# Optimization experiments

Hardware: AMD Instinct MI355X
Metric: run time of the kernel (lower is better)

Reference implementation:

```python
import jax, jax.numpy as jnp
import numpy as np

D = 512   # embed_dim
K = 8     # expand_dim
TAU = 16.0
LN_EPS = 1e-5


def setup_inputs() -> dict:
    key = jax.random.key(0)
    ks = jax.random.split(key, 8)
    b, n = 4, 4096
    x = jax.random.normal(ks[0], (b, n, D), dtype=jnp.float32)
    # nn.Linear weights stored as (in, out); bias=False everywhere
    W_i = jax.random.normal(ks[1], (D, D), dtype=jnp.float32) / np.sqrt(D)
    W_e = jax.random.normal(ks[2], (D, K), dtype=jnp.float32) / np.sqrt(D)
    W_s = jax.random.normal(ks[3], (D, K), dtype=jnp.float32) / np.sqrt(D)
    o_param = jax.random.normal(ks[4], (K, D), dtype=jnp.float32) * 0.1
    ln_gamma = jnp.ones((D,), dtype=jnp.float32)
    ln_beta = jnp.zeros((D,), dtype=jnp.float32)
    W_out = jax.random.normal(ks[5], (D, D), dtype=jnp.float32) / np.sqrt(D)
    return {"x": x, "W_i": W_i, "W_e": W_e, "W_s": W_s, "o_param": o_param,
            "ln_gamma": ln_gamma, "ln_beta": ln_beta, "W_out": W_out}


def reference(x, W_i, W_e, W_s, o_param, ln_gamma, ln_beta, W_out):
    b, n, d = x.shape
    k = W_e.shape[1]
    i = x @ W_i            # (b,n,d) input branch
    e = x @ W_e            # (b,n,k) expand branch (t_type=0: identity)
    s = x @ W_s            # (b,n,k) shrink branch
    # data-independent decay gate: exp(logsigmoid(o)/tau), shape (k,d)
    o = jnp.exp(jax.nn.log_sigmoid(o_param) / TAU)

    def step(m, inp):
        it, et, st = inp          # (b,d), (b,k), (b,k)
        m = o * m + et[:, :, None] * it[:, None, :]   # (b,k,d)
        y = jnp.einsum('bk,bkd->bd', st, m)
        return m, y

    m0 = jnp.zeros((b, k, d), dtype=x.dtype)
    xs = (jnp.swapaxes(i, 0, 1), jnp.swapaxes(e, 0, 1), jnp.swapaxes(s, 0, 1))
    _, ys = jax.lax.scan(step, m0, xs)   # ys: (n,b,d)
    y = jnp.swapaxes(ys, 0, 1)           # (b,n,d)
    # LayerNorm
    mu = jnp.mean(y, axis=-1, keepdims=True)
    var = jnp.mean(jnp.square(y - mu), axis=-1, keepdims=True)
    y = (y - mu) * jax.lax.rsqrt(var + LN_EPS) * ln_gamma + ln_beta
    return y @ W_out
```

## Files before the change

kernel.cpp:

```cpp
#include <hip/hip_runtime.h>
#include <stdint.h>

typedef __bf16 bf16;
typedef __bf16 bf16x8 __attribute__((ext_vector_type(8)));
typedef float  f32x4  __attribute__((ext_vector_type(4)));

#define NSEQ 4096
#define NROWS 16384
#define CHUNK 32
#define NCHUNKS_B 128
#define NCHUNKS 512
#define SEGLEN 16
#define NSEG 8
#define YSTRIDE 516

__device__ __forceinline__ float bf2f(uint16_t u){
    uint32_t w = ((uint32_t)u) << 16;
    return __builtin_bit_cast(float, w);
}
__device__ __forceinline__ uint32_t pack2(float a, float b){
    uint16_t ua = __builtin_bit_cast(uint16_t, (bf16)a);
    uint16_t ub = __builtin_bit_cast(uint16_t, (bf16)b);
    return ((uint32_t)ub << 16) | (uint32_t)ua;
}
__device__ __forceinline__ uint4 cvt8(const float* p){
    float4 lo = *(const float4*)p;
    float4 hi = *(const float4*)(p + 4);
    uint4 r;
    r.x = pack2(lo.x, lo.y); r.y = pack2(lo.z, lo.w);
    r.z = pack2(hi.x, hi.y); r.w = pack2(hi.z, hi.w);
    return r;
}
__device__ __forceinline__ float rd_any(const void* p, long idx, int f){
    return f ? ((const float*)p)[idx] : (float)((const bf16*)p)[idx];
}
__device__ __forceinline__ void cp16(const void* g, void* l){
    __builtin_amdgcn_global_load_lds((const __attribute__((address_space(1))) void*)g,
                                     (__attribute__((address_space(3))) void*)l,
                                     16, 0, 0);
}

__global__ __launch_bounds__(256) void prep_kernel(const uint32_t* __restrict__ xw,
                                                   const void* We, const void* Ws,
                                                   const void* op, const void* g, const void* b,
                                                   bf16* __restrict__ Wt_es,
                                                   float* __restrict__ g_c, float* __restrict__ b_c,
                                                   float* __restrict__ o_buf, float* __restrict__ oL_buf,
                                                   float* __restrict__ lsL_buf, float* __restrict__ oL16_buf,
                                                   int* __restrict__ flag_g){
    __shared__ int cnt[256];
    int tid = threadIdx.x;
    int c = 0;
    #pragma unroll
    for (int j = 0; j < 4; ++j){
        uint32_t w = xw[tid*4 + j];
        uint32_t e = (w >> 7) & 0xFF;
        c += (e >= 110 && e <= 140) ? 1 : 0;
    }
    cnt[tid] = c; __syncthreads();
    for (int s = 128; s; s >>= 1){
        if (tid < s) cnt[tid] += cnt[tid + s];
        __syncthreads();
    }
    int f = (cnt[0] < 512) ? 1 : 0;
    int blk = blockIdx.x;
    if (blk == 0 && tid == 0) flag_g[0] = f;
    if (blk < 8){
        for (int i = tid; i < 1024; i += 256){
            int gi = blk*1024 + i;
            int n = gi >> 9, k = gi & 511;
            float v = (n < 8) ? rd_any(We, (long)k*8 + n, f)
                              : rd_any(Ws, (long)k*8 + (n-8), f);
            Wt_es[gi] = (bf16)v;
        }
    } else {
        int base = (blk - 8) * 1024;
        for (int i = tid; i < 1024; i += 256){
            int gi = base + i;
            float x = rd_any(op, gi, f);
            float ls = (x < 0.f) ? (x - log1pf(expf(x))) : (0.f - log1pf(expf(-x)));
            o_buf[gi]    = expf(ls * (1.0f/16.0f));
            oL_buf[gi]   = expf(ls * 2.0f);
            lsL_buf[gi]  = ls * 2.0f;
            oL16_buf[gi] = expf(ls * 32.0f);
        }
    }
    if (blk == 0){
        for (int i = tid; i < 512; i += 256){
            g_c[i] = rd_any(g, i, f);
            b_c[i] = rd_any(b, i, f);
        }
    }
}

__global__ __launch_bounds__(256) void transpose2(const void* __restrict__ Wi,
                                                  const void* __restrict__ Wo,
                                                  bf16* __restrict__ Wt_i,
                                                  bf16* __restrict__ Wt_o,
                                                  const int* __restrict__ flag){
    __shared__ bf16 T[64][65];
    int mat = blockIdx.x >> 6;
    int t   = blockIdx.x & 63;
    int k0  = (t >> 3) * 64, n0 = (t & 7) * 64;
    const void* in = mat ? Wo : Wi;
    bf16* out = mat ? Wt_o : Wt_i;
    int f = *flag;
    int tid = threadIdx.x;
    #pragma unroll
    for (int e = 0; e < 16; ++e){
        int idx = e*256 + tid;
        int r = idx >> 6, c = idx & 63;
        T[c][r] = (bf16)rd_any(in, (long)(k0 + r)*512 + n0 + c, f);
    }
    __syncthreads();
    #pragma unroll
    for (int e = 0; e < 16; ++e){
        int idx = e*256 + tid;
        int rn = idx >> 6, ck = idx & 63;
        out[(long)(n0 + rn)*512 + k0 + ck] = T[rn][ck];
    }
}

__global__ __launch_bounds__(256) void gemm_bt(const void* __restrict__ Avoid,
                                               const bf16* __restrict__ Bt,
                                               void* __restrict__ Cvoid,
                                               int M, int N, int Kd,
                                               const int* __restrict__ aflag,
                                               const int* __restrict__ cflag,
                                               const bf16* __restrict__ Wes,
                                               float* __restrict__ e_out,
                                               float* __restrict__ s_out){
    __shared__ __align__(16) bf16 As[128*32];
    __shared__ __align__(16) bf16 Bs[128*32];
    const int tid  = threadIdx.x;
    const int lane = tid & 63;
    const int wave = tid >> 6;
    const int ntiles = N >> 7;
    int bid = blockIdx.x;
    {
        const int q = gridDim.x >> 3;
        bid = (bid & 7) * q + (bid >> 3);
    }
    const int mtile = bid / ntiles;
    const int ntile = bid - mtile*ntiles;
    const int m0 = mtile << 7, n0 = ntile << 7;
    const int wr = (wave >> 1) << 6;
    const int wc = (wave & 1) << 6;
    const int lrow = lane & 15;
    const int quad = lane >> 4;
    const int fa = aflag ? *aflag : 0;
    const bool do_es = (Wes != nullptr) && (ntile == 0) && (wc == 0);

    f32x4 acc[4][4] = {};
    f32x4 acc_es[4] = {};

    const int sr = tid >> 2;
    const int sk = (tid & 3) << 3;
    const bf16*  Ag  = (const bf16*) Avoid + (long)(m0 + sr)*Kd + sk;
    const float* Agf = (const float*)Avoid + (long)(m0 + sr)*Kd + sk;
    const bf16*  Bg  = Bt + (long)(n0 + sr)*Kd + sk;

    for (int k0 = 0; k0 < Kd; k0 += 32){
        uint4 a0, a1;
        if (fa){
            a0 = cvt8(Agf + k0);
            a1 = cvt8(Agf + (long)64*Kd + k0);
        }
        if (k0) __syncthreads();
        if (fa){
            *(uint4*)&As[tid*8]        = a0;
            *(uint4*)&As[2048 + tid*8] = a1;
        } else {
            cp16(Ag + k0,                &As[(size_t)wave*512]);
            cp16(Ag + (long)64*Kd + k0,  &As[2048 + (size_t)wave*512]);
        }
        cp16(Bg + k0,                &Bs[(size_t)wave*512]);
        cp16(Bg + (long)64*Kd + k0,  &Bs[2048 + (size_t)wave*512]);
        __syncthreads();

        bf16x8 af[4], bfr[4];
        #pragma unroll
        for (int i = 0; i < 4; ++i)
            af[i]  = *(const bf16x8*)&As[(wr + i*16 + lrow)*32 + quad*8];
        #pragma unroll
        for (int j = 0; j < 4; ++j)
            bfr[j] = *(const bf16x8*)&Bs[(wc + j*16 + lrow)*32 + quad*8];
        #pragma unroll
        for (int i = 0; i < 4; ++i)
            #pragma unroll
            for (int j = 0; j < 4; ++j)
                acc[i][j] = __builtin_amdgcn_mfma_f32_16x16x32_bf16(af[i], bfr[j], acc[i][j], 0, 0, 0);
        if (do_es){
            bf16x8 be = *(const bf16x8*)(Wes + (long)lrow*512 + k0 + quad*8);
            #pragma unroll
            for (int i = 0; i < 4; ++i)
                acc_es[i] = __builtin_amdgcn_mfma_f32_16x16x32_bf16(af[i], be, acc_es[i], 0, 0, 0);
        }
    }

    const int fc = cflag ? *cflag : 0;
    if (fc){
        float* Cf = (float*)Cvoid;
        #pragma unroll
        for (int i = 0; i < 4; ++i){
            int gr = m0 + wr + i*16 + quad*4;
            #pragma unroll
            for (int j = 0; j < 4; ++j){
                int gc = n0 + wc + j*16 + lrow;
                #pragma unroll
                for (int r = 0; r < 4; ++r)
                    Cf[(long)(gr + r)*N + gc] = acc[i][j][r];
            }
        }
    } else {
        bf16* Cb = (bf16*)Cvoid;
        #pragma unroll
        for (int i = 0; i < 4; ++i){
            int gr = m0 + wr + i*16 + quad*4;
            #pragma unroll
            for (int j = 0; j < 4; ++j){
                int gc = n0 + wc + j*16 + lrow;
                #pragma unroll
                for (int r = 0; r < 4; ++r)
                    Cb[(long)(gr + r)*N + gc] = (bf16)acc[i][j][r];
            }
        }
    }
    if (do_es){
        float* eo = (lrow < 8) ? e_out : s_out;
        int col = lrow & 7;
        #pragma unroll
        for (int i = 0; i < 4; ++i){
            int gr = m0 + wr + i*16 + quad*4;
            #pragma unroll
            for (int r = 0; r < 4; ++r)
                eo[(long)(gr + r)*8 + col] = acc_es[i][r];
        }
    }
}

__global__ __launch_bounds__(256) void passA(const bf16* __restrict__ i_buf,
                                             const float* __restrict__ e_buf,
                                             const float* __restrict__ o_buf,
                                             float* __restrict__ Ams){
    int c  = blockIdx.x;
    int b  = c >> 7;
    int t0 = (c & 127) * CHUNK;
    int tid = threadIdx.x;
    __shared__ float eS[CHUNK*8];
    eS[tid] = e_buf[((long)(b*NSEQ + t0))*8 + tid];
    __syncthreads();
    int d0 = tid*2;
    float o0[8], o1[8], m0[8], m1[8];
    #pragma unroll
    for (int k = 0; k < 8; ++k){
        o0[k] = o_buf[k*512 + d0]; o1[k] = o_buf[k*512 + d0 + 1];
        m0[k] = 0.f; m1[k] = 0.f;
    }
    const bf16* ip = i_buf + (long)(b*NSEQ + t0)*512 + d0;
    for (int t = 0; t < CHUNK; ++t){
        uint32_t iv = *(const uint32_t*)(ip + (long)t*512);
        float i0 = bf2f((uint16_t)iv), i1 = bf2f((uint16_t)(iv >> 16));
        #pragma unroll
        for (int k = 0; k < 8; ++k){
            float ek = eS[t*8 + k];
            m0[k] = o0[k]*m0[k] + ek*i0;
            m1[k] = o1[k]*m1[k] + ek*i1;
        }
    }
    float* Ac = Ams + (long)c*4096;
    #pragma unroll
    for (int k = 0; k < 8; ++k){
        float2 v; v.x = m0[k]; v.y = m1[k];
        *(float2*)&Ac[k*512 + d0] = v;
    }
}

__global__ __launch_bounds__(256) void passB1(float* __restrict__ Ams,
                                              const float* __restrict__ oL_buf,
                                              float* __restrict__ Tbuf){
    int bs  = blockIdx.x >> 4;
    int b   = bs >> 3, seg = bs & 7;
    int idx = (blockIdx.x & 15)*256 + threadIdx.x;
    float oL = oL_buf[idx];
    float m = 0.f;
    float* Mb = Ams + ((long)b*NCHUNKS_B + seg*SEGLEN)*4096 + idx;
    #pragma unroll 4
    for (int cc = 0; cc < SEGLEN; ++cc){
        float a = Mb[(long)cc*4096];
        Mb[(long)cc*4096] = m;
        m = oL*m + a;
    }
    Tbuf[(long)bs*4096 + idx] = m;
}

__global__ __launch_bounds__(256) void passB2(float* __restrict__ Tbuf,
                                              const float* __restrict__ oL16_buf){
    int b   = blockIdx.x >> 4;
    int idx = (blockIdx.x & 15)*256 + threadIdx.x;
    float oL16 = oL16_buf[idx];
    float t[NSEG];
    #pragma unroll
    for (int s = 0; s < NSEG; ++s)
        t[s] = Tbuf[((long)b*NSEG + s)*4096 + idx];
    float m = 0.f;
    #pragma unroll
    for (int s = 0; s < NSEG; ++s){
        Tbuf[((long)b*NSEG + s)*4096 + idx] = m;
        m = oL16*m + t[s];
    }
}

__global__ __launch_bounds__(256) void passC(bf16* __restrict__ iy,
                                             const float* __restrict__ e_buf,
                                             const float* __restrict__ s_buf,
                                             const float* __restrict__ o_buf,
                                             const float* __restrict__ Ploc,
                                             const float* __restrict__ Mseg,
                                             const float* __restrict__ lsL_buf,
                                             const float* __restrict__ g_c,
                                             const float* __restrict__ b_c){
    int c  = blockIdx.x;
    int b  = c >> 7;
    int cI = c & 127;
    int seg = cI >> 4;
    float fj = (float)(cI & 15);
    int t0 = cI * CHUNK;
    int tid = threadIdx.x;
    __shared__ float eS[CHUNK*8], sS[CHUNK*8];
    __shared__ float muS[CHUNK], rS[CHUNK];
    __shared__ __align__(16) float yS[CHUNK][YSTRIDE];
    eS[tid] = e_buf[((long)(b*NSEQ + t0))*8 + tid];
    sS[tid] = s_buf[((long)(b*NSEQ + t0))*8 + tid];
    __syncthreads();
    int d0 = tid*2;
    float o0[8], o1[8], m0[8], m1[8];
    const float* P0 = Ploc + (long)c*4096;
    const float* Ms = Mseg + ((long)b*NSEG + seg)*4096;
    #pragma unroll
    for (int k = 0; k < 8; ++k){
        int i0 = k*512 + d0;
        o0[k] = o_buf[i0]; o1[k] = o_buf[i0 + 1];
        m0[k] = P0[i0]   + __expf(lsL_buf[i0]  *fj)*Ms[i0];
        m1[k] = P0[i0+1] + __expf(lsL_buf[i0+1]*fj)*Ms[i0+1];
    }
    bf16* ip = iy + (long)(b*NSEQ + t0)*512 + d0;
    for (int t = 0; t < CHUNK; ++t){
        uint32_t iv = *(const uint32_t*)(ip + (long)t*512);
        float i0 = bf2f((uint16_t)iv), i1 = bf2f((uint16_t)(iv >> 16));
        float y0 = 0.f, y1 = 0.f;
        #pragma unroll
        for (int k = 0; k < 8; ++k){
            float ek = eS[t*8 + k], sk = sS[t*8 + k];
            m0[k] = o0[k]*m0[k] + ek*i0;
            m1[k] = o1[k]*m1[k] + ek*i1;
            y0 += sk*m0[k];
            y1 += sk*m1[k];
        }
        float2 yv; yv.x = y0; yv.y = y1;
        *(float2*)&yS[t][d0] = yv;
    }
    __syncthreads();
    {
        int row = tid >> 3, sub = tid & 7;
        const float4* yr = (const float4*)&yS[row][sub*64];
        float s = 0.f, s2 = 0.f;
        #pragma unroll
        for (int j = 0; j < 16; ++j){
            float4 v = yr[j];
            s  += v.x + v.y + v.z + v.w;
            s2 += v.x*v.x + v.y*v.y + v.z*v.z + v.w*v.w;
        }
        s += __shfl_xor(s, 1); s2 += __shfl_xor(s2, 1);
        s += __shfl_xor(s, 2); s2 += __shfl_xor(s2, 2);
        s += __shfl_xor(s, 4); s2 += __shfl_xor(s2, 4);
        if (sub == 0){
            float mu  = s * (1.f/512.f);
            float var = s2 * (1.f/512.f) - mu*mu;
            muS[row] = mu;
            rS[row]  = rsqrtf(var + 1e-5f);
        }
    }
    __syncthreads();
    float g0 = g_c[d0], g1 = g_c[d0+1];
    float bb0 = b_c[d0], bb1 = b_c[d0+1];
    for (int t = 0; t < CHUNK; ++t){
        float mu = muS[t], r = rS[t];
        float2 yv = *(const float2*)&yS[t][d0];
        float a0 = (yv.x - mu)*r*g0 + bb0;
        float a1 = (yv.y - mu)*r*g1 + bb1;
        *(uint32_t*)(ip + (long)t*512) = pack2(a0, a1);
    }
}

extern "C" void kernel_launch(void* const* d_in, const int* in_sizes, int n_in,
                              void* d_out, int out_size, void* d_ws, size_t ws_size,
                              hipStream_t stream){
    const void* x    = d_in[0];
    const void* W_i  = d_in[1];
    const void* W_e  = d_in[2];
    const void* W_s  = d_in[3];
    const void* o_p  = d_in[4];
    const void* gmm  = d_in[5];
    const void* bta  = d_in[6];
    const void* W_o  = d_in[7];

    char* ws = (char*)d_ws;
    bf16*  Wt_i   = (bf16*) (ws + 0);
    float* Tbuf   = (float*)(ws + 0);
    bf16*  Wt_o   = (bf16*) (ws + 524288);
    bf16*  iy_buf = (bf16*) (ws + 1048576);
    float* e_buf  = (float*)(ws + 17825792);
    float* s_buf  = (float*)(ws + 18350080);
    float* o_buf  = (float*)(ws + 18874368);
    float* oL_buf = (float*)(ws + 18890752);
    float* lsL    = (float*)(ws + 18907136);
    float* oL16   = (float*)(ws + 18923520);
    float* Ams    = (float*)(ws + 18939904);
    bf16*  Wt_es  = (bf16*) (ws + 27328512);
    float* g_c    = (float*)(ws + 27344896);
    float* b_c    = (float*)(ws + 27346944);
    int*   flag   = (int*)  (ws + 27348992);

    prep_kernel<<<12,   256, 0, stream>>>((const uint32_t*)x, W_e, W_s, o_p, gmm, bta,
                                          Wt_es, g_c, b_c, o_buf, oL_buf, lsL, oL16, flag);
    transpose2 <<<128,  256, 0, stream>>>(W_i, W_o, Wt_i, Wt_o, flag);
    gemm_bt    <<<512,  256, 0, stream>>>(x, Wt_i, iy_buf, NROWS, 512, 512, flag, nullptr,
                                          Wt_es, e_buf, s_buf);
    passA      <<<NCHUNKS, 256, 0, stream>>>(iy_buf, e_buf, o_buf, Ams);
    passB1     <<<512,  256, 0, stream>>>(Ams, oL_buf, Tbuf);
    passB2     <<<64,   256, 0, stream>>>(Tbuf, oL16);
    passC      <<<NCHUNKS, 256, 0, stream>>>(iy_buf, e_buf, s_buf, o_buf, Ams, Tbuf, lsL,
                                             g_c, b_c);
    gemm_bt    <<<512,  256, 0, stream>>>(iy_buf, Wt_o, d_out, NROWS, 512, 512, nullptr, flag,
                                          nullptr, nullptr, nullptr);
}
```

Before: 177.2 us.

## Fuse chunked scan passes into one cooperative kernel and merge prep kernels

Merges the prep and weight-transpose kernels into a single launch. Replaces the four chunked-scan kernels (chunk-local state, two-level inter-chunk prefix, output+LayerNorm) with one cooperative kernel that uses grid.sync between phases. The chunk's iy tile stays in LDS across phases, so it is loaded from global memory once instead of twice. This trades launch gaps and reloads for grid-wide barriers and a co-residency requirement of 512 blocks, with a fallback to the old passes if the cooperative launch fails.

```diff
diff --git a/kernel.cpp b/kernel.cpp
--- a/kernel.cpp
+++ b/kernel.cpp
@@ -1,5 +1,8 @@
 #include <hip/hip_runtime.h>
+#include <hip/hip_cooperative_groups.h>
 #include <stdint.h>
+
+namespace cg = cooperative_groups;
 
 typedef __bf16 bf16;
 typedef __bf16 bf16x8 __attribute__((ext_vector_type(8)));
@@ -12,6 +15,7 @@
 #define NCHUNKS 512
 #define SEGLEN 16
 #define NSEG 8
+#define YST 520
 #define YSTRIDE 516
 
 __device__ __forceinline__ float bf2f(uint16_t u){
@@ -40,15 +44,19 @@
                                      16, 0, 0);
 }
 
-__global__ __launch_bounds__(256) void prep_kernel(const uint32_t* __restrict__ xw,
-                                                   const void* We, const void* Ws,
-                                                   const void* op, const void* g, const void* b,
-                                                   bf16* __restrict__ Wt_es,
-                                                   float* __restrict__ g_c, float* __restrict__ b_c,
-                                                   float* __restrict__ o_buf, float* __restrict__ oL_buf,
-                                                   float* __restrict__ lsL_buf, float* __restrict__ oL16_buf,
-                                                   int* __restrict__ flag_g){
+__global__ __launch_bounds__(256) void prep_all(const uint32_t* __restrict__ xw,
+                                                const void* __restrict__ Wi,
+                                                const void* __restrict__ Wo,
+                                                const void* We, const void* Ws,
+                                                const void* op, const void* g, const void* bta,
+                                                bf16* __restrict__ Wt_i, bf16* __restrict__ Wt_o,
+                                                bf16* __restrict__ Wt_es,
+                                                float* __restrict__ g_c, float* __restrict__ b_c,
+                                                float* __restrict__ o_buf, float* __restrict__ oL_buf,
+                                                float* __restrict__ lsL_buf, float* __restrict__ oL16_buf,
+                                                int* __restrict__ flag_g){
     __shared__ int cnt[256];
+    __shared__ bf16 T[64][65];
     int tid = threadIdx.x;
     int c = 0;
     #pragma unroll
@@ -65,16 +73,38 @@
     int f = (cnt[0] < 512) ? 1 : 0;
     int blk = blockIdx.x;
     if (blk == 0 && tid == 0) flag_g[0] = f;
-    if (blk < 8){
+
+    if (blk < 128){
+        int mat = blk >> 6;
+        int t   = blk & 63;
+        int k0  = (t >> 3) * 64, n0 = (t & 7) * 64;
+        const void* in = mat ? Wo : Wi;
+        bf16* out = mat ? Wt_o : Wt_i;
+        #pragma unroll
+        for (int e = 0; e < 16; ++e){
+            int idx = e*256 + tid;
+            int r = idx >> 6, cc = idx & 63;
+            T[cc][r] = (bf16)rd_any(in, (long)(k0 + r)*512 + n0 + cc, f);
+        }
+        __syncthreads();
+        #pragma unroll
+        for (int e = 0; e < 16; ++e){
+            int idx = e*256 + tid;
+            int rn = idx >> 6, ck = idx & 63;
+            out[(long)(n0 + rn)*512 + k0 + ck] = T[rn][ck];
+        }
+    } else if (blk < 136){
+        int sub = blk - 128;
         for (int i = tid; i < 1024; i += 256){
-            int gi = blk*1024 + i;
+            int gi = sub*1024 + i;
             int n = gi >> 9, k = gi & 511;
             float v = (n < 8) ? rd_any(We, (long)k*8 + n, f)
                               : rd_any(Ws, (long)k*8 + (n-8), f);
             Wt_es[gi] = (bf16)v;
         }
     } else {
-        int base = (blk - 8) * 1024;
+        int sub = blk - 136;
+        int base = sub * 1024;
         for (int i = tid; i < 1024; i += 256){
             int gi = base + i;
             float x = rd_any(op, gi, f);
@@ -84,40 +114,12 @@
             lsL_buf[gi]  = ls * 2.0f;
             oL16_buf[gi] = expf(ls * 32.0f);
         }
-    }
-    if (blk == 0){
-        for (int i = tid; i < 512; i += 256){
-            g_c[i] = rd_any(g, i, f);
-            b_c[i] = rd_any(b, i, f);
-        }
-    }
-}
-
-__global__ __launch_bounds__(256) void transpose2(const void* __restrict__ Wi,
-                                                  const void* __restrict__ Wo,
-                                                  bf16* __restrict__ Wt_i,
-                                                  bf16* __restrict__ Wt_o,
-                                                  const int* __restrict__ flag){
-    __shared__ bf16 T[64][65];
-    int mat = blockIdx.x >> 6;
-    int t   = blockIdx.x & 63;
-    int k0  = (t >> 3) * 64, n0 = (t & 7) * 64;
-    const void* in = mat ? Wo : Wi;
-    bf16* out = mat ? Wt_o : Wt_i;
-    int f = *flag;
-    int tid = threadIdx.x;
-    #pragma unroll
-    for (int e = 0; e < 16; ++e){
-        int idx = e*256 + tid;
-        int r = idx >> 6, c = idx & 63;
-        T[c][r] = (bf16)rd_any(in, (long)(k0 + r)*512 + n0 + c, f);
-    }
-    __syncthreads();
-    #pragma unroll
-    for (int e = 0; e < 16; ++e){
-        int idx = e*256 + tid;
-        int rn = idx >> 6, ck = idx & 63;
-        out[(long)(n0 + rn)*512 + k0 + ck] = T[rn][ck];
+        if (sub == 0){
+            for (int i = tid; i < 512; i += 256){
+                g_c[i] = rd_any(g, i, f);
+                b_c[i] = rd_any(bta, i, f);
+            }
+        }
     }
 }
 
@@ -235,6 +237,169 @@
             #pragma unroll
             for (int r = 0; r < 4; ++r)
                 eo[(long)(gr + r)*8 + col] = acc_es[i][r];
+        }
+    }
+}
+
+__global__ __launch_bounds__(256, 2) void scan_fused(bf16* __restrict__ iy,
+                                                     const float* __restrict__ e_buf,
+                                                     const float* __restrict__ s_buf,
+                                                     const float* __restrict__ o_buf,
+                                                     const float* __restrict__ oL_buf,
+                                                     const float* __restrict__ oL16_buf,
+                                                     const float* __restrict__ lsL_buf,
+                                                     float* __restrict__ Ams,
+                                                     float* __restrict__ Tbuf,
+                                                     const float* __restrict__ g_c,
+                                                     const float* __restrict__ b_c){
+    cg::grid_group grid = cg::this_grid();
+    const int c  = blockIdx.x;
+    const int b  = c >> 7;
+    const int cI = c & 127;
+    const int t0 = cI * CHUNK;
+    const int tid  = threadIdx.x;
+    const int lane = tid & 63;
+    const int wave = tid >> 6;
+
+    __shared__ __align__(16) bf16 iyS[CHUNK * YST];
+    __shared__ float eS[CHUNK*8], sS[CHUNK*8];
+    __shared__ float muS[CHUNK], rS[CHUNK];
+
+    bf16* gsrc = iy + ((long)(b*NSEQ + t0))*512;
+    #pragma unroll
+    for (int j = 0; j < 8; ++j){
+        int row = wave*8 + j;
+        cp16(gsrc + (long)row*512 + lane*8, &iyS[row*YST]);
+    }
+    eS[tid] = e_buf[((long)(b*NSEQ + t0))*8 + tid];
+    sS[tid] = s_buf[((long)(b*NSEQ + t0))*8 + tid];
+    __syncthreads();
+
+    const int d0 = tid*2;
+    float o0[8], o1[8], m0v[8], m1v[8];
+    #pragma unroll
+    for (int k = 0; k < 8; ++k){
+        o0[k] = o_buf[k*512 + d0]; o1[k] = o_buf[k*512 + d0 + 1];
+        m0v[k] = 0.f; m1v[k] = 0.f;
+    }
+    for (int t = 0; t < CHUNK; ++t){
+        uint32_t iv = *(const uint32_t*)&iyS[t*YST + d0];
+        float i0 = bf2f((uint16_t)iv), i1 = bf2f((uint16_t)(iv >> 16));
+        #pragma unroll
+        for (int k = 0; k < 8; ++k){
+            float ek = eS[t*8 + k];
+            m0v[k] = o0[k]*m0v[k] + ek*i0;
+            m1v[k] = o1[k]*m1v[k] + ek*i1;
+        }
+    }
+    {
+        float* Ac = Ams + (long)c*4096;
+        #pragma unroll
+        for (int k = 0; k < 8; ++k){
+            float2 v; v.x = m0v[k]; v.y = m1v[k];
+            *(float2*)&Ac[k*512 + d0] = v;
+        }
+    }
+    __threadfence();
+    grid.sync();
+
+    {
+        int bs  = c >> 4;
+        int b1  = bs >> 3, seg = bs & 7;
+        int idx = (c & 15)*256 + tid;
+        float oL = oL_buf[idx];
+        float m = 0.f;
+        float* Mb = Ams + ((long)b1*NCHUNKS_B + seg*SEGLEN)*4096 + idx;
+        #pragma unroll 4
+        for (int cc = 0; cc < SEGLEN; ++cc){
+            float a = Mb[(long)cc*4096];
+            Mb[(long)cc*4096] = m;
+            m = oL*m + a;
+        }
+        Tbuf[(long)bs*4096 + idx] = m;
+    }
+    __threadfence();
+    grid.sync();
+
+    if (c < 64){
+        int b2  = c >> 4;
+        int idx = (c & 15)*256 + tid;
+        float oL16 = oL16_buf[idx];
+        float t[NSEG];
+        #pragma unroll
+        for (int s = 0; s < NSEG; ++s)
+            t[s] = Tbuf[((long)b2*NSEG + s)*4096 + idx];
+        float m = 0.f;
+        #pragma unroll
+        for (int s = 0; s < NSEG; ++s){
+            Tbuf[((long)b2*NSEG + s)*4096 + idx] = m;
+            m = oL16*m + t[s];
+        }
+    }
+    __threadfence();
+    grid.sync();
+
+    {
+        int seg = cI >> 4;
+        float fj = (float)(cI & 15);
+        const float* P0 = Ams  + (long)c*4096;
+        const float* Ms = Tbuf + ((long)b*NSEG + seg)*4096;
+        #pragma unroll
+        for (int k = 0; k < 8; ++k){
+            int i0 = k*512 + d0;
+            m0v[k] = P0[i0]   + __expf(lsL_buf[i0]  *fj)*Ms[i0];
+            m1v[k] = P0[i0+1] + __expf(lsL_buf[i0+1]*fj)*Ms[i0+1];
+        }
+        for (int t = 0; t < CHUNK; ++t){
+            uint32_t iv = *(const uint32_t*)&iyS[t*YST + d0];
+            float i0 = bf2f((uint16_t)iv), i1 = bf2f((uint16_t)(iv >> 16));
+            float y0 = 0.f, y1 = 0.f;
+            #pragma unroll
+            for (int k = 0; k < 8; ++k){
+                float ek = eS[t*8 + k], sk = sS[t*8 + k];
+                m0v[k] = o0[k]*m0v[k] + ek*i0;
+                m1v[k] = o1[k]*m1v[k] + ek*i1;
+                y0 += sk*m0v[k];
+                y1 += sk*m1v[k];
+            }
+            *(uint32_t*)&iyS[t*YST + d0] = pack2(y0, y1);
+        }
+    }
+    __syncthreads();
+    #pragma unroll
+    for (int rr = 0; rr < 8; ++rr){
+        int row = wave*8 + rr;
+        uint4 u = *(const uint4*)&iyS[row*YST + lane*8];
+        const uint16_t* uu = (const uint16_t*)&u;
+        float s = 0.f, s2 = 0.f;
+        #pragma unroll
+        for (int j = 0; j < 8; ++j){
+            float v = bf2f(uu[j]);
+            s += v; s2 += v*v;
+        }
+        #pragma unroll
+        for (int off = 1; off < 64; off <<= 1){
+            s  += __shfl_xor(s, off);
+            s2 += __shfl_xor(s2, off);
+        }
+        if (lane == 0){
+            float mu  = s * (1.f/512.f);
+            float var = s2 * (1.f/512.f) - mu*mu;
+            muS[row] = mu;
+            rS[row]  = rsqrtf(var + 1e-5f);
+        }
+    }
+    __syncthreads();
+    {
+        float g0 = g_c[d0], g1 = g_c[d0+1];
+        float bb0 = b_c[d0], bb1 = b_c[d0+1];
+        bf16* ip = iy + (long)(b*NSEQ + t0)*512 + d0;
+        for (int t = 0; t < CHUNK; ++t){
+            float mu = muS[t], r = rS[t];
+            uint32_t yv = *(const uint32_t*)&iyS[t*YST + d0];
+            float a0 = (bf2f((uint16_t)yv)        - mu)*r*g0 + bb0;
+            float a1 = (bf2f((uint16_t)(yv >> 16)) - mu)*r*g1 + bb1;
+            *(uint32_t*)(ip + (long)t*512) = pack2(a0, a1);
         }
     }
 }
@@ -422,16 +587,24 @@
     float* b_c    = (float*)(ws + 27346944);
     int*   flag   = (int*)  (ws + 27348992);
 
-    prep_kernel<<<12,   256, 0, stream>>>((const uint32_t*)x, W_e, W_s, o_p, gmm, bta,
-                                          Wt_es, g_c, b_c, o_buf, oL_buf, lsL, oL16, flag);
-    transpose2 <<<128,  256, 0, stream>>>(W_i, W_o, Wt_i, Wt_o, flag);
-    gemm_bt    <<<512,  256, 0, stream>>>(x, Wt_i, iy_buf, NROWS, 512, 512, flag, nullptr,
-                                          Wt_es, e_buf, s_buf);
-    passA      <<<NCHUNKS, 256, 0, stream>>>(iy_buf, e_buf, o_buf, Ams);
-    passB1     <<<512,  256, 0, stream>>>(Ams, oL_buf, Tbuf);
-    passB2     <<<64,   256, 0, stream>>>(Tbuf, oL16);
-    passC      <<<NCHUNKS, 256, 0, stream>>>(iy_buf, e_buf, s_buf, o_buf, Ams, Tbuf, lsL,
-                                             g_c, b_c);
-    gemm_bt    <<<512,  256, 0, stream>>>(iy_buf, Wt_o, d_out, NROWS, 512, 512, nullptr, flag,
-                                          nullptr, nullptr, nullptr);
-}
+    prep_all<<<140, 256, 0, stream>>>((const uint32_t*)x, W_i, W_o, W_e, W_s, o_p, gmm, bta,
+                                      Wt_i, Wt_o, Wt_es, g_c, b_c, o_buf, oL_buf, lsL, oL16, flag);
+    gemm_bt <<<512, 256, 0, stream>>>(x, Wt_i, iy_buf, NROWS, 512, 512, flag, nullptr,
+                                      Wt_es, e_buf, s_buf);
+    {
+        void* args[] = { (void*)&iy_buf, (void*)&e_buf, (void*)&s_buf, (void*)&o_buf,
+                         (void*)&oL_buf, (void*)&oL16, (void*)&lsL, (void*)&Ams,
+                         (void*)&Tbuf, (void*)&g_c, (void*)&b_c };
+        hipError_t cerr = hipLaunchCooperativeKernel((const void*)scan_fused, dim3(NCHUNKS),
+                                                     dim3(256), args, 0, stream);
+        if (cerr != hipSuccess){
+            passA <<<NCHUNKS, 256, 0, stream>>>(iy_buf, e_buf, o_buf, Ams);
+            passB1<<<512,    256, 0, stream>>>(Ams, oL_buf, Tbuf);
+            passB2<<<64,     256, 0, stream>>>(Tbuf, oL16);
+            passC <<<NCHUNKS, 256, 0, stream>>>(iy_buf, e_buf, s_buf, o_buf, Ams, Tbuf, lsL,
+                                                g_c, b_c);
+        }
+    }
+    gemm_bt <<<512, 256, 0, stream>>>(iy_buf, Wt_o, d_out, NROWS, 512, 512, nullptr, flag,
+                                      nullptr, nullptr, nullptr);
+}
```

New measurement: 488.9 us. 176% more time.

## Double-buffer GEMM LDS tiles and merge weight transpose into prep kernel

Applied to the files above, without the earlier changes.

The GEMM main loop now uses two LDS buffers and issues the next K-slice's global loads (async LDS copies, or fp32 register loads for the converted path) before computing on the current slice. This overlaps memory latency with MFMA work and needs one barrier per iteration instead of two. Separately, the weight transpose kernel is folded into the prep kernel, removing one launch and the flag round-trip through memory. The cost is double the LDS use per block, which could lower occupancy, plus extra registers for the prefetched fp32 values.

```diff
diff --git a/kernel.cpp b/kernel.cpp
--- a/kernel.cpp
+++ b/kernel.cpp
@@ -40,15 +40,19 @@
                                      16, 0, 0);
 }
 
-__global__ __launch_bounds__(256) void prep_kernel(const uint32_t* __restrict__ xw,
-                                                   const void* We, const void* Ws,
-                                                   const void* op, const void* g, const void* b,
-                                                   bf16* __restrict__ Wt_es,
-                                                   float* __restrict__ g_c, float* __restrict__ b_c,
-                                                   float* __restrict__ o_buf, float* __restrict__ oL_buf,
-                                                   float* __restrict__ lsL_buf, float* __restrict__ oL16_buf,
-                                                   int* __restrict__ flag_g){
+__global__ __launch_bounds__(256) void prep_all(const uint32_t* __restrict__ xw,
+                                                const void* __restrict__ Wi,
+                                                const void* __restrict__ Wo,
+                                                const void* We, const void* Ws,
+                                                const void* op, const void* g, const void* bta,
+                                                bf16* __restrict__ Wt_i, bf16* __restrict__ Wt_o,
+                                                bf16* __restrict__ Wt_es,
+                                                float* __restrict__ g_c, float* __restrict__ b_c,
+                                                float* __restrict__ o_buf, float* __restrict__ oL_buf,
+                                                float* __restrict__ lsL_buf, float* __restrict__ oL16_buf,
+                                                int* __restrict__ flag_g){
     __shared__ int cnt[256];
+    __shared__ bf16 T[64][65];
     int tid = threadIdx.x;
     int c = 0;
     #pragma unroll
@@ -65,16 +69,38 @@
     int f = (cnt[0] < 512) ? 1 : 0;
     int blk = blockIdx.x;
     if (blk == 0 && tid == 0) flag_g[0] = f;
-    if (blk < 8){
+
+    if (blk < 128){
+        int mat = blk >> 6;
+        int t   = blk & 63;
+        int k0  = (t >> 3) * 64, n0 = (t & 7) * 64;
+        const void* in = mat ? Wo : Wi;
+        bf16* out = mat ? Wt_o : Wt_i;
+        #pragma unroll
+        for (int e = 0; e < 16; ++e){
+            int idx = e*256 + tid;
+            int r = idx >> 6, cc = idx & 63;
+            T[cc][r] = (bf16)rd_any(in, (long)(k0 + r)*512 + n0 + cc, f);
+        }
+        __syncthreads();
+        #pragma unroll
+        for (int e = 0; e < 16; ++e){
+            int idx = e*256 + tid;
+            int rn = idx >> 6, ck = idx & 63;
+            out[(long)(n0 + rn)*512 + k0 + ck] = T[rn][ck];
+        }
+    } else if (blk < 136){
+        int sub = blk - 128;
         for (int i = tid; i < 1024; i += 256){
-            int gi = blk*1024 + i;
+            int gi = sub*1024 + i;
             int n = gi >> 9, k = gi & 511;
             float v = (n < 8) ? rd_any(We, (long)k*8 + n, f)
                               : rd_any(Ws, (long)k*8 + (n-8), f);
             Wt_es[gi] = (bf16)v;
         }
     } else {
-        int base = (blk - 8) * 1024;
+        int sub = blk - 136;
+        int base = sub * 1024;
         for (int i = tid; i < 1024; i += 256){
             int gi = base + i;
             float x = rd_any(op, gi, f);
@@ -84,40 +110,12 @@
             lsL_buf[gi]  = ls * 2.0f;
             oL16_buf[gi] = expf(ls * 32.0f);
         }
-    }
-    if (blk == 0){
-        for (int i = tid; i < 512; i += 256){
-            g_c[i] = rd_any(g, i, f);
-            b_c[i] = rd_any(b, i, f);
-        }
-    }
-}
-
-__global__ __launch_bounds__(256) void transpose2(const void* __restrict__ Wi,
-                                                  const void* __restrict__ Wo,
-                                                  bf16* __restrict__ Wt_i,
-                                                  bf16* __restrict__ Wt_o,
-                                                  const int* __restrict__ flag){
-    __shared__ bf16 T[64][65];
-    int mat = blockIdx.x >> 6;
-    int t   = blockIdx.x & 63;
-    int k0  = (t >> 3) * 64, n0 = (t & 7) * 64;
-    const void* in = mat ? Wo : Wi;
-    bf16* out = mat ? Wt_o : Wt_i;
-    int f = *flag;
-    int tid = threadIdx.x;
-    #pragma unroll
-    for (int e = 0; e < 16; ++e){
-        int idx = e*256 + tid;
-        int r = idx >> 6, c = idx & 63;
-        T[c][r] = (bf16)rd_any(in, (long)(k0 + r)*512 + n0 + c, f);
-    }
-    __syncthreads();
-    #pragma unroll
-    for (int e = 0; e < 16; ++e){
-        int idx = e*256 + tid;
-        int rn = idx >> 6, ck = idx & 63;
-        out[(long)(n0 + rn)*512 + k0 + ck] = T[rn][ck];
+        if (sub == 0){
+            for (int i = tid; i < 512; i += 256){
+                g_c[i] = rd_any(g, i, f);
+                b_c[i] = rd_any(bta, i, f);
+            }
+        }
     }
 }
 
@@ -130,8 +128,8 @@
                                                const bf16* __restrict__ Wes,
                                                float* __restrict__ e_out,
                                                float* __restrict__ s_out){
-    __shared__ __align__(16) bf16 As[128*32];
-    __shared__ __align__(16) bf16 Bs[128*32];
+    __shared__ __align__(16) bf16 As[2][128*32];
+    __shared__ __align__(16) bf16 Bs[2][128*32];
     const int tid  = threadIdx.x;
     const int lane = tid & 63;
     const int wave = tid >> 6;
@@ -160,31 +158,44 @@
     const float* Agf = (const float*)Avoid + (long)(m0 + sr)*Kd + sk;
     const bf16*  Bg  = Bt + (long)(n0 + sr)*Kd + sk;
 
+    if (fa){
+        *(uint4*)&As[0][tid*8]        = cvt8(Agf);
+        *(uint4*)&As[0][2048 + tid*8] = cvt8(Agf + (long)64*Kd);
+    } else {
+        cp16(Ag,                 &As[0][(size_t)wave*512]);
+        cp16(Ag + (long)64*Kd,   &As[0][2048 + (size_t)wave*512]);
+    }
+    cp16(Bg,               &Bs[0][(size_t)wave*512]);
+    cp16(Bg + (long)64*Kd, &Bs[0][2048 + (size_t)wave*512]);
+    __syncthreads();
+
+    int cur = 0;
     for (int k0 = 0; k0 < Kd; k0 += 32){
-        uint4 a0, a1;
-        if (fa){
-            a0 = cvt8(Agf + k0);
-            a1 = cvt8(Agf + (long)64*Kd + k0);
-        }
-        if (k0) __syncthreads();
-        if (fa){
-            *(uint4*)&As[tid*8]        = a0;
-            *(uint4*)&As[2048 + tid*8] = a1;
-        } else {
-            cp16(Ag + k0,                &As[(size_t)wave*512]);
-            cp16(Ag + (long)64*Kd + k0,  &As[2048 + (size_t)wave*512]);
-        }
-        cp16(Bg + k0,                &Bs[(size_t)wave*512]);
-        cp16(Bg + (long)64*Kd + k0,  &Bs[2048 + (size_t)wave*512]);
-        __syncthreads();
+        const int nxt  = cur ^ 1;
+        const int k1   = k0 + 32;
+        const bool more = (k1 < Kd);
+        float4 la0, la1, lb0, lb1;
+        if (more){
+            if (fa){
+                la0 = *(const float4*)(Agf + k1);
+                la1 = *(const float4*)(Agf + k1 + 4);
+                lb0 = *(const float4*)(Agf + (long)64*Kd + k1);
+                lb1 = *(const float4*)(Agf + (long)64*Kd + k1 + 4);
+            } else {
+                cp16(Ag + k1,               &As[nxt][(size_t)wave*512]);
+                cp16(Ag + (long)64*Kd + k1, &As[nxt][2048 + (size_t)wave*512]);
+            }
+            cp16(Bg + k1,               &Bs[nxt][(size_t)wave*512]);
+            cp16(Bg + (long)64*Kd + k1, &Bs[nxt][2048 + (size_t)wave*512]);
+        }
 
         bf16x8 af[4], bfr[4];
         #pragma unroll
         for (int i = 0; i < 4; ++i)
-            af[i]  = *(const bf16x8*)&As[(wr + i*16 + lrow)*32 + quad*8];
+            af[i]  = *(const bf16x8*)&As[cur][(wr + i*16 + lrow)*32 + quad*8];
         #pragma unroll
         for (int j = 0; j < 4; ++j)
-            bfr[j] = *(const bf16x8*)&Bs[(wc + j*16 + lrow)*32 + quad*8];
+            bfr[j] = *(const bf16x8*)&Bs[cur][(wc + j*16 + lrow)*32 + quad*8];
         #pragma unroll
         for (int i = 0; i < 4; ++i)
             #pragma unroll
@@ -196,6 +207,18 @@
             for (int i = 0; i < 4; ++i)
                 acc_es[i] = __builtin_amdgcn_mfma_f32_16x16x32_bf16(af[i], be, acc_es[i], 0, 0, 0);
         }
+
+        if (more && fa){
+            uint4 A0, A1;
+            A0.x = pack2(la0.x, la0.y); A0.y = pack2(la0.z, la0.w);
+            A0.z = pack2(la1.x, la1.y); A0.w = pack2(la1.z, la1.w);
+            A1.x = pack2(lb0.x, lb0.y); A1.y = pack2(lb0.z, lb0.w);
+            A1.z = pack2(lb1.x, lb1.y); A1.w = pack2(lb1.z, lb1.w);
+            *(uint4*)&As[nxt][tid*8]        = A0;
+            *(uint4*)&As[nxt][2048 + tid*8] = A1;
+        }
+        __syncthreads();
+        cur = nxt;
     }
 
     const int fc = cflag ? *cflag : 0;
@@ -422,16 +445,15 @@
     float* b_c    = (float*)(ws + 27346944);
     int*   flag   = (int*)  (ws + 27348992);
 
-    prep_kernel<<<12,   256, 0, stream>>>((const uint32_t*)x, W_e, W_s, o_p, gmm, bta,
-                                          Wt_es, g_c, b_c, o_buf, oL_buf, lsL, oL16, flag);
-    transpose2 <<<128,  256, 0, stream>>>(W_i, W_o, Wt_i, Wt_o, flag);
-    gemm_bt    <<<512,  256, 0, stream>>>(x, Wt_i, iy_buf, NROWS, 512, 512, flag, nullptr,
-                                          Wt_es, e_buf, s_buf);
-    passA      <<<NCHUNKS, 256, 0, stream>>>(iy_buf, e_buf, o_buf, Ams);
-    passB1     <<<512,  256, 0, stream>>>(Ams, oL_buf, Tbuf);
-    passB2     <<<64,   256, 0, stream>>>(Tbuf, oL16);
-    passC      <<<NCHUNKS, 256, 0, stream>>>(iy_buf, e_buf, s_buf, o_buf, Ams, Tbuf, lsL,
-                                             g_c, b_c);
-    gemm_bt    <<<512,  256, 0, stream>>>(iy_buf, Wt_o, d_out, NROWS, 512, 512, nullptr, flag,
-                                          nullptr, nullptr, nullptr);
-}
+    prep_all<<<140, 256, 0, stream>>>((const uint32_t*)x, W_i, W_o, W_e, W_s, o_p, gmm, bta,
+                                      Wt_i, Wt_o, Wt_es, g_c, b_c, o_buf, oL_buf, lsL, oL16, flag);
+    gemm_bt <<<512, 256, 0, stream>>>(x, Wt_i, iy_buf, NROWS, 512, 512, flag, nullptr,
+                                      Wt_es, e_buf, s_buf);
+    passA  <<<NCHUNKS, 256, 0, stream>>>(iy_buf, e_buf, o_buf, Ams);
+    passB1 <<<512,  256, 0, stream>>>(Ams, oL_buf, Tbuf);
+    passB2 <<<64,   256, 0, stream>>>(Tbuf, oL16);
+    passC  <<<NCHUNKS, 256, 0, stream>>>(iy_buf, e_buf, s_buf, o_buf, Ams, Tbuf, lsL,
+                                         g_c, b_c);
+    gemm_bt <<<512, 256, 0, stream>>>(iy_buf, Wt_o, d_out, NROWS, 512, 512, nullptr, flag,
+                                      nullptr, nullptr, nullptr);
+}
```

New measurement: 174.8 us. No clear change (-1.4%).
